# Performance work log

Hardware: AMD Instinct MI355X
Metric: run time of the kernel (lower is better)

The kernel has to match this reference:

```python
import jax, jax.numpy as jnp
import numpy as np

N_NODES = 100000
N_EDGES = 1600000
N_GRAPHS = 512
NFEAT = 64
HIDDEN = 128
NTARGETS = 16
TIME_DIM = 128
NLAYERS = 3  # conv1 + 2 extra convs


def setup_inputs() -> dict:
    key = jax.random.key(0)
    ks = jax.random.split(key, 12)
    x = jax.random.normal(ks[0], (N_NODES, NFEAT), dtype=jnp.float32)
    edge_index = jax.random.randint(ks[1], (2, N_EDGES), 0, N_NODES, dtype=jnp.int64)
    t_embedding = jax.random.normal(ks[2], (N_NODES, TIME_DIM), dtype=jnp.float32)
    batch = jnp.sort(jax.random.randint(ks[3], (N_NODES,), 0, N_GRAPHS, dtype=jnp.int64))
    s = lambda k, shp, fan_in: jax.random.normal(k, shp, jnp.float32) * (1.0 / np.sqrt(fan_in))
    Wt = s(ks[4], (TIME_DIM, HIDDEN), TIME_DIM)
    bt = jnp.zeros((HIDDEN,), jnp.float32)
    W1 = s(ks[5], (NFEAT, HIDDEN), NFEAT)
    b1 = jnp.zeros((HIDDEN,), jnp.float32)
    Ws = s(ks[6], (NLAYERS - 1, HIDDEN, HIDDEN), HIDDEN)
    bs = jnp.zeros((NLAYERS - 1, HIDDEN), jnp.float32)
    Wo = s(ks[7], (HIDDEN, NTARGETS), HIDDEN)
    bo = jnp.zeros((NTARGETS,), jnp.float32)
    return {"x": x, "edge_index": edge_index, "t_embedding": t_embedding,
            "batch": batch, "Wt": Wt, "bt": bt, "W1": W1, "b1": b1,
            "Ws": Ws, "bs": bs, "Wo": Wo, "bo": bo}


def _gcn_conv(h, src, dst, norm, W, b, n_nodes):
    # PyG GCNConv: h' = scatter_add(norm * (h @ W)[src] -> dst) + b
    h = h @ W                                   # [N, out]
    msg = h[src] * norm[:, None]                # [E+N, out]
    agg = jax.ops.segment_sum(msg, dst, num_segments=n_nodes)
    return agg + b


def reference(x, edge_index, t_embedding, batch, Wt, bt, W1, b1, Ws, bs, Wo, bo):
    n = x.shape[0]
    # add self-loops (static shapes)
    loop = jnp.arange(n, dtype=edge_index.dtype)
    src = jnp.concatenate([edge_index[0], loop])
    dst = jnp.concatenate([edge_index[1], loop])
    # symmetric normalization D^-1/2 (A+I) D^-1/2
    deg = jax.ops.segment_sum(jnp.ones(dst.shape[0], x.dtype), dst, num_segments=n)
    dinv = jnp.where(deg > 0, jax.lax.rsqrt(deg), 0.0)
    norm = dinv[src] * dinv[dst]                # [E+N]

    t_emb = jax.nn.relu(t_embedding @ Wt + bt)  # time_mlp
    h = jax.nn.relu(_gcn_conv(x, src, dst, norm, W1, b1, n)) + t_emb
    for i in range(Ws.shape[0]):
        h = jax.nn.relu(_gcn_conv(h, src, dst, norm, Ws[i], bs[i], n))

    # global mean pool over graphs
    gsum = jax.ops.segment_sum(h, batch, num_segments=N_GRAPHS)
    cnt = jax.ops.segment_sum(jnp.ones(n, h.dtype), batch, num_segments=N_GRAPHS)
    pooled = gsum / jnp.maximum(cnt, 1.0)[:, None]
    return pooled @ Wo + bo
```

## Files before the change

### kernel.cpp

```cpp
#include <hip/hip_runtime.h>

#define N_NODES  100000
#define N_EDGES  1600000
#define N_GRAPHS 512
#define HID      128
#define NB       196
#define NCHUNK   196
#define CHUNK    8192
#define ECAP     512

typedef unsigned int  uint;
typedef unsigned char uchar;
typedef unsigned short ushort;
typedef __attribute__((ext_vector_type(8))) short  short8;
typedef __attribute__((ext_vector_type(4))) float  f32x4;
typedef __attribute__((ext_vector_type(2))) float  f32x2;

__device__ inline float bflo(uint u) { return __uint_as_float(u << 16); }
__device__ inline float bfhi(uint u) { return __uint_as_float(u & 0xffff0000u); }
__device__ inline ushort f2bf(float f) {
    uint u = __float_as_uint(f);
    return (ushort)((u + 0x7fffu + ((u >> 16) & 1u)) >> 16);
}
__device__ inline uint pk(float a, float b) {
    return (uint)f2bf(a) | ((uint)f2bf(b) << 16);
}

__device__ inline void acc16_fp8(uint4 hv, float w, float* a) {
    f32x2 p;
    p = __builtin_amdgcn_cvt_pk_f32_fp8((int)hv.x, false); a[0]  += w * p.x; a[1]  += w * p.y;
    p = __builtin_amdgcn_cvt_pk_f32_fp8((int)hv.x, true);  a[2]  += w * p.x; a[3]  += w * p.y;
    p = __builtin_amdgcn_cvt_pk_f32_fp8((int)hv.y, false); a[4]  += w * p.x; a[5]  += w * p.y;
    p = __builtin_amdgcn_cvt_pk_f32_fp8((int)hv.y, true);  a[6]  += w * p.x; a[7]  += w * p.y;
    p = __builtin_amdgcn_cvt_pk_f32_fp8((int)hv.z, false); a[8]  += w * p.x; a[9]  += w * p.y;
    p = __builtin_amdgcn_cvt_pk_f32_fp8((int)hv.z, true);  a[10] += w * p.x; a[11] += w * p.y;
    p = __builtin_amdgcn_cvt_pk_f32_fp8((int)hv.w, false); a[12] += w * p.x; a[13] += w * p.y;
    p = __builtin_amdgcn_cvt_pk_f32_fp8((int)hv.w, true);  a[14] += w * p.x; a[15] += w * p.y;
}

__global__ __launch_bounds__(256)
void prep_kernel(const float* __restrict__ Wt, const float* __restrict__ W1,
                 const float* __restrict__ Ws, ushort* __restrict__ packed,
                 const int* __restrict__ batch, int* __restrict__ gstart,
                 const float* __restrict__ temb, ushort* __restrict__ tembb) {
    int b = blockIdx.x;
    int t = threadIdx.x;
    if (b < 224) {
        int tid = b * 256 + t;
        const float* src; int p; ushort* dst;
        if (tid < 16384)      { src = Wt;         p = tid;         dst = packed; }
        else if (tid < 24576) { src = W1;         p = tid - 16384; dst = packed + 16384; }
        else if (tid < 40960) { src = Ws;         p = tid - 24576; dst = packed + 24576; }
        else                  { src = Ws + 16384; p = tid - 40960; dst = packed + 40960; }
        int j  = p & 7;
        int L  = (p >> 3) & 63;
        int cb = (p >> 9) & 7;
        int s  = p >> 12;
        int k  = s * 32 + (L >> 4) * 8 + j;
        int n  = cb * 16 + (L & 15);
        dst[p] = f2bf(src[k * 128 + n]);
    } else if (b < 615) {
        int i = (b - 224) * 256 + t;
        if (i >= N_NODES) return;
        int bb = batch[i];
        int prev = (i == 0) ? -1 : batch[i - 1];
        for (int g = prev + 1; g <= bb; ++g) gstart[g] = i;
        if (i == N_NODES - 1) {
            for (int g = bb + 1; g <= N_GRAPHS; ++g) gstart[g] = N_NODES;
        }
    } else {
        long i = ((long)(b - 615) * 256 + t) * 16;
#pragma unroll
        for (int k = 0; k < 4; ++k) {
            float4 f = *(const float4*)(temb + i + k * 4);
            uint2 o; o.x = pk(f.x, f.y); o.y = pk(f.z, f.w);
            *(uint2*)(tembb + i + k * 4) = o;
        }
    }
}


__global__ __launch_bounds__(256)
void hist_chunks(const int* __restrict__ dst, int* __restrict__ chunk_hist) {
    __shared__ int h[NB];
    int c = blockIdx.x, t = threadIdx.x;
    if (t < NB) h[t] = 0;
    __syncthreads();
    const int4* d4 = (const int4*)dst;
#pragma unroll
    for (int k = 0; k < 8; ++k) {
        int i4 = c * (CHUNK / 4) + k * 256 + t;
        if (i4 < N_EDGES / 4) {
            int4 d = d4[i4];
            atomicAdd(&h[d.x >> 9], 1);
            atomicAdd(&h[d.y >> 9], 1);
            atomicAdd(&h[d.z >> 9], 1);
            atomicAdd(&h[d.w >> 9], 1);
        }
    }
    __syncthreads();
    if (t < NB) chunk_hist[c * NB + t] = h[t];
}

__global__ __launch_bounds__(256)
void scan_chunks(const int* __restrict__ chunk_hist, int* __restrict__ cbase,
                 int* __restrict__ bstart, int* __restrict__ row_ptr) {
    __shared__ int sc[256];
    int t = threadIdx.x;
    int tot = 0;
    if (t < NB)
        for (int c = 0; c < NCHUNK; ++c) tot += chunk_hist[c * NB + t];
    sc[t] = (t < NB) ? tot : 0;
    __syncthreads();
    for (int off = 1; off < 256; off <<= 1) {
        int x = (t >= off) ? sc[t - off] : 0;
        __syncthreads();
        sc[t] += x;
        __syncthreads();
    }
    int excl = sc[t] - ((t < NB) ? tot : 0);
    if (t < NB) {
        bstart[t] = excl;
        int run = excl;
        for (int c = 0; c < NCHUNK; ++c) {
            cbase[c * NB + t] = run;
            run += chunk_hist[c * NB + t];
        }
    }
    if (t == 0) { bstart[NB] = N_EDGES; row_ptr[N_NODES] = N_EDGES; }
}

__global__ __launch_bounds__(256)
void scatter_coarse(const int* __restrict__ src, const int* __restrict__ dst,
                    const int* __restrict__ cbase, uint* __restrict__ tmp) {
    __shared__ int cur[NB];
    int c = blockIdx.x, t = threadIdx.x;
    if (t < NB) cur[t] = cbase[c * NB + t];
    __syncthreads();
    const int4* s4p = (const int4*)src;
    const int4* d4p = (const int4*)dst;
#pragma unroll
    for (int k = 0; k < 8; ++k) {
        int i4 = c * (CHUNK / 4) + k * 256 + t;
        if (i4 < N_EDGES / 4) {
            int4 s = s4p[i4];
            int4 d = d4p[i4];
            int p;
            p = atomicAdd(&cur[d.x >> 9], 1); tmp[p] = (uint)s.x | (((uint)(d.x & 511)) << 17);
            p = atomicAdd(&cur[d.y >> 9], 1); tmp[p] = (uint)s.y | (((uint)(d.y & 511)) << 17);
            p = atomicAdd(&cur[d.z >> 9], 1); tmp[p] = (uint)s.z | (((uint)(d.z & 511)) << 17);
            p = atomicAdd(&cur[d.w >> 9], 1); tmp[p] = (uint)s.w | (((uint)(d.w & 511)) << 17);
        }
    }
}

__global__ __launch_bounds__(256)
void csr_fine(const uint* __restrict__ tmp, const int* __restrict__ bstart,
              int* __restrict__ row_ptr, float* __restrict__ dinv,
              int* __restrict__ edge, const float* __restrict__ x,
              uchar* __restrict__ xb8) {
    __shared__ int   cnt[512];
    __shared__ float dvloc[512];
    __shared__ int   ps[256];
    int b = blockIdx.x, t = threadIdx.x;
    int node0 = b << 9;
    int ncnt = min(512, N_NODES - node0);
    int s = bstart[b], e = bstart[b + 1];
    cnt[t] = 0; cnt[t + 256] = 0;
    __syncthreads();
    for (int i = s + t; i < e; i += 256) atomicAdd(&cnt[tmp[i] >> 17], 1);
    __syncthreads();
    int c0 = cnt[2 * t], c1 = cnt[2 * t + 1];
    int pair = c0 + c1;
    ps[t] = pair;
    __syncthreads();
    for (int off = 1; off < 256; off <<= 1) {
        int v = (t >= off) ? ps[t - off] : 0;
        __syncthreads();
        ps[t] += v;
        __syncthreads();
    }
    int ep = ps[t] - pair;
    int p0 = s + ep, p1 = s + ep + c0;
    float dv0 = rsqrtf((float)(c0 + 1));
    float dv1 = rsqrtf((float)(c1 + 1));
    int n0 = node0 + 2 * t;
    if (2 * t < ncnt)     { row_ptr[n0]     = p0; dinv[n0]     = dv0; }
    if (2 * t + 1 < ncnt) { row_ptr[n0 + 1] = p1; dinv[n0 + 1] = dv1; }
    dvloc[2 * t] = dv0; dvloc[2 * t + 1] = dv1;
    cnt[2 * t] = p0; cnt[2 * t + 1] = p1;
    __syncthreads();
    for (int i = s + t; i < e; i += 256) {
        uint rec = tmp[i];
        int p = atomicAdd(&cnt[rec >> 17], 1);
        edge[p] = (int)(rec & 0x1FFFFu);
    }
    for (int idx = t; idx < ncnt * 16; idx += 256) {
        int row = idx >> 4, q = idx & 15;
        float4 f = ((const float4*)(x + (size_t)(node0 + row) * 64))[q];
        float d = dvloc[row];
        int w = __builtin_amdgcn_cvt_pk_fp8_f32(f.x * d, f.y * d, 0, false);
        w     = __builtin_amdgcn_cvt_pk_fp8_f32(f.z * d, f.w * d, w, true);
        *(uint*)(xb8 + (size_t)(node0 + row) * 64 + q * 4) = (uint)w;
    }
}

template <int K, bool TEMB, bool OUT8, bool SCALEOUT>
__global__ __launch_bounds__(256)
void fused_conv(const void* __restrict__ Hv, const int* __restrict__ rp,
                const int* __restrict__ edge, const float* __restrict__ dinv,
                const ushort* __restrict__ Wp, const float* __restrict__ bias,
                const ushort* __restrict__ tembb, const ushort* __restrict__ Wtp,
                const float* __restrict__ bias_t, void* __restrict__ Ov, int ntiles) {
    constexpr int LPR  = K / 16;
    constexpr int G    = 64 / LPR;
    constexpr int RPG  = 16 / G;
    constexpr int U    = 8;
    constexpr int LROW = 136;
    __shared__ __align__(16) ushort sA[4][16 * LROW];
    __shared__ uint sE[4][ECAP];
    const int wave = threadIdx.x >> 6;
    const int lane = threadIdx.x & 63;
    const int tile = blockIdx.x * 4 + wave;
    if (tile >= ntiles) return;
    const int row0 = tile * 16;
    const int g  = lane / LPR;
    const int fq = lane % LPR;
    ushort* myA = sA[wave];
    const uchar* H8 = (const uchar*)Hv;

    int   rpv = rp[row0 + ((lane < 17) ? lane : 16)];
    float dvv = dinv[row0 + ((lane < 16) ? lane : 15)];

    const int s0   = __shfl(rpv, 0);
    const int e15  = __shfl(rpv, 16);
    const int ecnt = e15 - s0;
    uint* sEw = sE[wave];
    for (int i = lane; i < ecnt && i < ECAP; i += 64)
        sEw[i] = ((const uint*)edge)[s0 + i];

    auto phase1 = [&](auto eload) {
        for (int rr = 0; rr < RPG; ++rr) {
            int r = g * RPG + rr;
            int v = row0 + r;
            int s = __shfl(rpv, r), e = __shfl(rpv, r + 1);
            float a[16];
            {
                uint4 xv = *(const uint4*)(H8 + (size_t)v * K + fq * 16);
                f32x2 p;
                p = __builtin_amdgcn_cvt_pk_f32_fp8((int)xv.x, false); a[0]  = p.x; a[1]  = p.y;
                p = __builtin_amdgcn_cvt_pk_f32_fp8((int)xv.x, true);  a[2]  = p.x; a[3]  = p.y;
                p = __builtin_amdgcn_cvt_pk_f32_fp8((int)xv.y, false); a[4]  = p.x; a[5]  = p.y;
                p = __builtin_amdgcn_cvt_pk_f32_fp8((int)xv.y, true);  a[6]  = p.x; a[7]  = p.y;
                p = __builtin_amdgcn_cvt_pk_f32_fp8((int)xv.z, false); a[8]  = p.x; a[9]  = p.y;
                p = __builtin_amdgcn_cvt_pk_f32_fp8((int)xv.z, true);  a[10] = p.x; a[11] = p.y;
                p = __builtin_amdgcn_cvt_pk_f32_fp8((int)xv.w, false); a[12] = p.x; a[13] = p.y;
                p = __builtin_amdgcn_cvt_pk_f32_fp8((int)xv.w, true);  a[14] = p.x; a[15] = p.y;
            }
            int iters = (e - s + U - 1) / U;
            int j = s;
            for (int i = 0; i < iters; ++i, j += U) {
                int sv[U]; float wv[U];
#pragma unroll
                for (int u = 0; u < U; ++u) {
                    int jv = j + u;
                    int jj = (jv < e) ? jv : e - 1;
                    sv[u] = eload(jj);
                    wv[u] = (jv < e) ? 1.0f : 0.0f;
                }
                uint4 hv[U];
#pragma unroll
                for (int u = 0; u < U; ++u)
                    hv[u] = *(const uint4*)(H8 + (size_t)sv[u] * K + fq * 16);
#pragma unroll
                for (int u = 0; u < U; ++u) acc16_fp8(hv[u], wv[u], a);
            }
            float dv = __shfl(dvv, r);
            uint4 o1, o2;
            o1.x = pk(a[0] * dv,  a[1] * dv);  o1.y = pk(a[2] * dv,  a[3] * dv);
            o1.z = pk(a[4] * dv,  a[5] * dv);  o1.w = pk(a[6] * dv,  a[7] * dv);
            o2.x = pk(a[8] * dv,  a[9] * dv);  o2.y = pk(a[10] * dv, a[11] * dv);
            o2.z = pk(a[12] * dv, a[13] * dv); o2.w = pk(a[14] * dv, a[15] * dv);
            *(uint4*)(myA + r * LROW + fq * 16)     = o1;
            *(uint4*)(myA + r * LROW + fq * 16 + 8) = o2;
        }
    };
    if (ecnt <= ECAP) {
        phase1([&](int jj) { return (int)sEw[jj - s0]; });
    } else {
        phase1([&](int jj) { return (int)((const uint*)edge)[jj]; });
    }

    const int m = lane & 15, q = lane >> 4;
    f32x4 acc[8];
#pragma unroll
    for (int cb = 0; cb < 8; ++cb) acc[cb] = {0.f, 0.f, 0.f, 0.f};
    constexpr int S = K / 32;
#pragma unroll
    for (int s = 0; s < S; ++s) {
        short8 av = *(const short8*)(myA + m * LROW + s * 32 + q * 8);
#pragma unroll
        for (int cb = 0; cb < 8; ++cb) {
            short8 b = *(const short8*)(Wp + (size_t)((s * 8 + cb) * 64 + lane) * 8);
            acc[cb] = __builtin_amdgcn_mfma_f32_16x16x32_bf16(av, b, acc[cb], 0, 0, 0);
        }
    }

    f32x4 acc2[TEMB ? 8 : 1];
    if constexpr (TEMB) {
#pragma unroll
        for (int cb = 0; cb < 8; ++cb) acc2[cb] = {0.f, 0.f, 0.f, 0.f};
        const ushort* Arow = tembb + (size_t)(row0 + m) * 128 + q * 8;
#pragma unroll
        for (int s2 = 0; s2 < 4; ++s2) {
            short8 av = *(const short8*)(Arow + s2 * 32);
#pragma unroll
            for (int cb = 0; cb < 8; ++cb) {
                short8 b = *(const short8*)(Wtp + (size_t)((s2 * 8 + cb) * 64 + lane) * 8);
                acc2[cb] = __builtin_amdgcn_mfma_f32_16x16x32_bf16(av, b, acc2[cb], 0, 0, 0);
            }
        }
    }

    float dsc[4];
    if constexpr (SCALEOUT) {
#pragma unroll
        for (int r = 0; r < 4; ++r) dsc[r] = __shfl(dvv, q * 4 + r);
    }
    if constexpr (!OUT8) {
        ushort* Ob = (ushort*)Ov;
#pragma unroll
        for (int cb = 0; cb < 8; ++cb) {
            int colc = cb * 16 + m;
            float bv = bias[colc];
            float bt2 = TEMB ? bias_t[colc] : 0.f;
#pragma unroll
            for (int r = 0; r < 4; ++r) {
                int row = q * 4 + r;
                float v = fmaxf(acc[cb][r] + bv, 0.0f);
                if (TEMB) v += fmaxf(acc2[cb][r] + bt2, 0.0f);
                if (SCALEOUT) v *= dsc[r];
                myA[row * LROW + colc] = f2bf(v);
            }
        }
#pragma unroll
        for (int i = 0; i < 4; ++i) {
            int srow = i * 4 + (lane >> 4);
            int scol = (lane & 15) * 8;
            *(short8*)(Ob + (size_t)(row0 + srow) * 128 + scol) =
                *(const short8*)(myA + srow * LROW + scol);
        }
    } else {
        uchar* st8 = (uchar*)myA;
        uchar* Ob = (uchar*)Ov;
#pragma unroll
        for (int cb = 0; cb < 8; ++cb) {
            int colc = cb * 16 + m;
            float bv = bias[colc];
            float bt2 = TEMB ? bias_t[colc] : 0.f;
#pragma unroll
            for (int r = 0; r < 4; ++r) {
                int row = q * 4 + r;
                float v = fmaxf(acc[cb][r] + bv, 0.0f);
                if (TEMB) v += fmaxf(acc2[cb][r] + bt2, 0.0f);
                if (SCALEOUT) v *= dsc[r];
                int enc = __builtin_amdgcn_cvt_pk_fp8_f32(v, v, 0, false);
                st8[row * 136 + colc] = (uchar)(enc & 0xff);
            }
        }
#pragma unroll
        for (int i = 0; i < 4; ++i) {
            int idx = i * 64 + lane;
            int srow = idx >> 4;
            int soff = (idx & 15) * 8;
            *(uint2*)(Ob + (size_t)(row0 + srow) * 128 + soff) =
                *(const uint2*)(st8 + srow * 136 + soff);
        }
    }
}


__global__ void pool_out(const ushort* __restrict__ h, const int* __restrict__ gstart,
                         const float* __restrict__ Wo, const float* __restrict__ bo,
                         float* __restrict__ out) {
    int g = blockIdx.x;
    int t = threadIdx.x;
    int f4 = t & 31;
    int sl = t >> 5;
    int s = gstart[g], e = gstart[g + 1];
    float a0 = 0.f, a1 = 0.f, a2 = 0.f, a3 = 0.f;
    for (int i = s + sl; i < e; i += 8) {
        uint2 u = *(const uint2*)(h + (size_t)i * HID + f4 * 4);
        a0 += bflo(u.x); a1 += bfhi(u.x);
        a2 += bflo(u.y); a3 += bfhi(u.y);
    }
    __shared__ float red[256][4];
    __shared__ float P[128];
    red[t][0] = a0; red[t][1] = a1; red[t][2] = a2; red[t][3] = a3;
    __syncthreads();
    if (sl == 0) {
        for (int k = 1; k < 8; ++k) {
            a0 += red[f4 + 32 * k][0]; a1 += red[f4 + 32 * k][1];
            a2 += red[f4 + 32 * k][2]; a3 += red[f4 + 32 * k][3];
        }
        float c = (float)((e - s) < 1 ? 1 : (e - s));
        P[f4 * 4]     = a0 / c; P[f4 * 4 + 1] = a1 / c;
        P[f4 * 4 + 2] = a2 / c; P[f4 * 4 + 3] = a3 / c;
    }
    __syncthreads();
    if (t < 16) {
        float acc = bo[t];
        for (int k = 0; k < HID; ++k) acc += P[k] * Wo[k * 16 + t];
        out[g * 16 + t] = acc;
    }
}


extern "C" void kernel_launch(void* const* d_in, const int* in_sizes, int n_in,
                              void* d_out, int out_size, void* d_ws, size_t ws_size,
                              hipStream_t stream) {
    const float* x       = (const float*)d_in[0];
    const int*   ei      = (const int*)d_in[1];
    const float* temb_in = (const float*)d_in[2];
    const int*   batch   = (const int*)d_in[3];
    const float* Wt      = (const float*)d_in[4];
    const float* bt      = (const float*)d_in[5];
    const float* W1      = (const float*)d_in[6];
    const float* b1      = (const float*)d_in[7];
    const float* Ws      = (const float*)d_in[8];
    const float* bs      = (const float*)d_in[9];
    const float* Wo      = (const float*)d_in[10];
    const float* bo      = (const float*)d_in[11];
    float* out = (float*)d_out;

    const int N = N_NODES, E = N_EDGES;
    const int* src = ei;
    const int* dst = ei + E;

    char* p = (char*)d_ws;
    auto carve = [&](size_t bytes) -> void* {
        void* r = (void*)p;
        p += (bytes + 255) & ~(size_t)255;
        return r;
    };
    int*    row_ptr    = (int*)carve((size_t)(N + 1) * 4);
    float*  dinv       = (float*)carve((size_t)N * 4);
    int*    gstart     = (int*)carve((size_t)(N_GRAPHS + 1) * 4);
    ushort* packed     = (ushort*)carve((size_t)57344 * 2);
    int*    chunk_hist = (int*)carve((size_t)NCHUNK * NB * 4);
    int*    cbase      = (int*)carve((size_t)NCHUNK * NB * 4);
    int*    bstart     = (int*)carve((size_t)(NB + 1) * 4);
    uint*   tmp        = (uint*)carve((size_t)E * 4);
    int*    edge       = (int*)carve((size_t)E * 4);
    uchar*  xb8        = (uchar*)carve((size_t)(N + 16) * 64);
    ushort* tembb      = (ushort*)carve((size_t)N * 128 * 2);
    uchar*  H1f8       = (uchar*)carve((size_t)(N + 16) * 128);
    uchar*  H2f8       = (uchar*)carve((size_t)(N + 16) * 128);
    ushort* H3         = (ushort*)carve((size_t)N * 128 * 2);

    const ushort* Wtp  = packed;
    const ushort* W1p  = packed + 16384;
    const ushort* Ws0p = packed + 24576;
    const ushort* Ws1p = packed + 40960;

    const int ntiles = N / 16;
    const int gblk   = (ntiles + 3) / 4;

    prep_kernel<<<3740, 256, 0, stream>>>(Wt, W1, Ws, packed, batch, gstart,
                                          temb_in, tembb);

    hist_chunks<<<NCHUNK, 256, 0, stream>>>(dst, chunk_hist);
    scan_chunks<<<1, 256, 0, stream>>>(chunk_hist, cbase, bstart, row_ptr);
    scatter_coarse<<<NCHUNK, 256, 0, stream>>>(src, dst, cbase, tmp);
    csr_fine<<<NB, 256, 0, stream>>>(tmp, bstart, row_ptr, dinv, edge, x, xb8);

    fused_conv<64, true, true, true><<<gblk, 256, 0, stream>>>(
        xb8, row_ptr, edge, dinv, W1p, b1, tembb, Wtp, bt, H1f8, ntiles);
    fused_conv<128, false, true, true><<<gblk, 256, 0, stream>>>(
        H1f8, row_ptr, edge, dinv, Ws0p, bs, nullptr, nullptr, nullptr, H2f8, ntiles);
    fused_conv<128, false, false, false><<<gblk, 256, 0, stream>>>(
        H2f8, row_ptr, edge, dinv, Ws1p, bs + 128, nullptr, nullptr, nullptr, H3, ntiles);

    pool_out<<<N_GRAPHS, 256, 0, stream>>>(H3, gstart, Wo, bo, out);
}
```

Baseline: 367.9 us.

## Fuse pooling into last conv, merge histogram into prep, refine CSR buckets

Several changes land together. The edge histogram moves into the prep kernel, and the coarse bucket count grows from 196 to 782 buckets of 128 nodes. The single serial scan becomes a parallel two-level scan over a transposed layout. The last conv now reduces its tile rows per graph and accumulates them into a float pooled buffer with atomics, which removes the bf16 H3 write, the pool_out read and one launch. The cost is global atomic contention on pooled and more blocks in csr_fine, each using only half its threads.

```diff
diff --git a/kernel.cpp b/kernel.cpp
--- a/kernel.cpp
+++ b/kernel.cpp
@@ -4,7 +4,7 @@
 #define N_EDGES  1600000
 #define N_GRAPHS 512
 #define HID      128
-#define NB       196
+#define NB       782
 #define NCHUNK   196
 #define CHUNK    8192
 #define ECAP     512
@@ -42,23 +42,26 @@
 void prep_kernel(const float* __restrict__ Wt, const float* __restrict__ W1,
                  const float* __restrict__ Ws, ushort* __restrict__ packed,
                  const int* __restrict__ batch, int* __restrict__ gstart,
-                 const float* __restrict__ temb, ushort* __restrict__ tembb) {
+                 const float* __restrict__ temb, ushort* __restrict__ tembb,
+                 const int* __restrict__ dst, int* __restrict__ chunk_hist,
+                 float* __restrict__ pooled) {
+    __shared__ int h[NB];
     int b = blockIdx.x;
     int t = threadIdx.x;
     if (b < 224) {
         int tid = b * 256 + t;
-        const float* src; int p; ushort* dst;
-        if (tid < 16384)      { src = Wt;         p = tid;         dst = packed; }
-        else if (tid < 24576) { src = W1;         p = tid - 16384; dst = packed + 16384; }
-        else if (tid < 40960) { src = Ws;         p = tid - 24576; dst = packed + 24576; }
-        else                  { src = Ws + 16384; p = tid - 40960; dst = packed + 40960; }
+        const float* src; int p; ushort* dstp;
+        if (tid < 16384)      { src = Wt;         p = tid;         dstp = packed; }
+        else if (tid < 24576) { src = W1;         p = tid - 16384; dstp = packed + 16384; }
+        else if (tid < 40960) { src = Ws;         p = tid - 24576; dstp = packed + 24576; }
+        else                  { src = Ws + 16384; p = tid - 40960; dstp = packed + 40960; }
         int j  = p & 7;
         int L  = (p >> 3) & 63;
         int cb = (p >> 9) & 7;
         int s  = p >> 12;
         int k  = s * 32 + (L >> 4) * 8 + j;
         int n  = cb * 16 + (L & 15);
-        dst[p] = f2bf(src[k * 128 + n]);
+        dstp[p] = f2bf(src[k * 128 + n]);
     } else if (b < 615) {
         int i = (b - 224) * 256 + t;
         if (i >= N_NODES) return;
@@ -68,7 +71,7 @@
         if (i == N_NODES - 1) {
             for (int g = bb + 1; g <= N_GRAPHS; ++g) gstart[g] = N_NODES;
         }
-    } else {
+    } else if (b < 3740) {
         long i = ((long)(b - 615) * 256 + t) * 16;
 #pragma unroll
         for (int k = 0; k < 4; ++k) {
@@ -76,41 +79,61 @@
             uint2 o; o.x = pk(f.x, f.y); o.y = pk(f.z, f.w);
             *(uint2*)(tembb + i + k * 4) = o;
         }
-    }
-}
-
-
-__global__ __launch_bounds__(256)
-void hist_chunks(const int* __restrict__ dst, int* __restrict__ chunk_hist) {
-    __shared__ int h[NB];
-    int c = blockIdx.x, t = threadIdx.x;
-    if (t < NB) h[t] = 0;
-    __syncthreads();
-    const int4* d4 = (const int4*)dst;
-#pragma unroll
-    for (int k = 0; k < 8; ++k) {
-        int i4 = c * (CHUNK / 4) + k * 256 + t;
-        if (i4 < N_EDGES / 4) {
-            int4 d = d4[i4];
-            atomicAdd(&h[d.x >> 9], 1);
-            atomicAdd(&h[d.y >> 9], 1);
-            atomicAdd(&h[d.z >> 9], 1);
-            atomicAdd(&h[d.w >> 9], 1);
-        }
-    }
-    __syncthreads();
-    if (t < NB) chunk_hist[c * NB + t] = h[t];
-}
-
-__global__ __launch_bounds__(256)
-void scan_chunks(const int* __restrict__ chunk_hist, int* __restrict__ cbase,
-                 int* __restrict__ bstart, int* __restrict__ row_ptr) {
+    } else if (b < 3936) {
+        int c = b - 3740;
+        for (int i = t; i < NB; i += 256) h[i] = 0;
+        __syncthreads();
+        const int4* d4 = (const int4*)dst;
+#pragma unroll
+        for (int k = 0; k < 8; ++k) {
+            int i4 = c * (CHUNK / 4) + k * 256 + t;
+            if (i4 < N_EDGES / 4) {
+                int4 d = d4[i4];
+                atomicAdd(&h[d.x >> 7], 1);
+                atomicAdd(&h[d.y >> 7], 1);
+                atomicAdd(&h[d.z >> 7], 1);
+                atomicAdd(&h[d.w >> 7], 1);
+            }
+        }
+        __syncthreads();
+        for (int i = t; i < NB; i += 256) chunk_hist[c * NB + i] = h[i];
+    } else {
+        pooled[(b - 3936) * 256 + t] = 0.f;
+    }
+}
+
+
+__global__ __launch_bounds__(256)
+void scanA(const int* __restrict__ chunk_hist, int* __restrict__ cbaseT,
+           int* __restrict__ btotal) {
+    __shared__ int sc[256];
+    int b = blockIdx.x, t = threadIdx.x;
+    int v = (t < NCHUNK) ? chunk_hist[t * NB + b] : 0;
+    sc[t] = v;
+    __syncthreads();
+    for (int off = 1; off < 256; off <<= 1) {
+        int x = (t >= off) ? sc[t - off] : 0;
+        __syncthreads();
+        sc[t] += x;
+        __syncthreads();
+    }
+    if (t < NCHUNK) cbaseT[b * NCHUNK + t] = sc[t] - v;
+    if (t == 255) btotal[b] = sc[255];
+}
+
+__global__ __launch_bounds__(256)
+void scanB(const int* __restrict__ btotal, int* __restrict__ bstart,
+           int* __restrict__ row_ptr) {
     __shared__ int sc[256];
     int t = threadIdx.x;
-    int tot = 0;
-    if (t < NB)
-        for (int c = 0; c < NCHUNK; ++c) tot += chunk_hist[c * NB + t];
-    sc[t] = (t < NB) ? tot : 0;
+    int v[4]; int sum = 0;
+#pragma unroll
+    for (int k = 0; k < 4; ++k) {
+        int idx = t * 4 + k;
+        v[k] = (idx < NB) ? btotal[idx] : 0;
+        sum += v[k];
+    }
+    sc[t] = sum;
     __syncthreads();
     for (int off = 1; off < 256; off <<= 1) {
         int x = (t >= off) ? sc[t - off] : 0;
@@ -118,24 +141,23 @@
         sc[t] += x;
         __syncthreads();
     }
-    int excl = sc[t] - ((t < NB) ? tot : 0);
-    if (t < NB) {
-        bstart[t] = excl;
-        int run = excl;
-        for (int c = 0; c < NCHUNK; ++c) {
-            cbase[c * NB + t] = run;
-            run += chunk_hist[c * NB + t];
-        }
+    int run = sc[t] - sum;
+#pragma unroll
+    for (int k = 0; k < 4; ++k) {
+        int idx = t * 4 + k;
+        if (idx < NB) bstart[idx] = run;
+        run += v[k];
     }
     if (t == 0) { bstart[NB] = N_EDGES; row_ptr[N_NODES] = N_EDGES; }
 }
 
 __global__ __launch_bounds__(256)
 void scatter_coarse(const int* __restrict__ src, const int* __restrict__ dst,
-                    const int* __restrict__ cbase, uint* __restrict__ tmp) {
+                    const int* __restrict__ cbaseT, const int* __restrict__ bstart,
+                    uint* __restrict__ tmp) {
     __shared__ int cur[NB];
     int c = blockIdx.x, t = threadIdx.x;
-    if (t < NB) cur[t] = cbase[c * NB + t];
+    for (int i = t; i < NB; i += 256) cur[i] = cbaseT[i * NCHUNK + c] + bstart[i];
     __syncthreads();
     const int4* s4p = (const int4*)src;
     const int4* d4p = (const int4*)dst;
@@ -146,10 +168,10 @@
             int4 s = s4p[i4];
             int4 d = d4p[i4];
             int p;
-            p = atomicAdd(&cur[d.x >> 9], 1); tmp[p] = (uint)s.x | (((uint)(d.x & 511)) << 17);
-            p = atomicAdd(&cur[d.y >> 9], 1); tmp[p] = (uint)s.y | (((uint)(d.y & 511)) << 17);
-            p = atomicAdd(&cur[d.z >> 9], 1); tmp[p] = (uint)s.z | (((uint)(d.z & 511)) << 17);
-            p = atomicAdd(&cur[d.w >> 9], 1); tmp[p] = (uint)s.w | (((uint)(d.w & 511)) << 17);
+            p = atomicAdd(&cur[d.x >> 7], 1); tmp[p] = (uint)s.x | (((uint)(d.x & 127)) << 17);
+            p = atomicAdd(&cur[d.y >> 7], 1); tmp[p] = (uint)s.y | (((uint)(d.y & 127)) << 17);
+            p = atomicAdd(&cur[d.z >> 7], 1); tmp[p] = (uint)s.z | (((uint)(d.z & 127)) << 17);
+            p = atomicAdd(&cur[d.w >> 7], 1); tmp[p] = (uint)s.w | (((uint)(d.w & 127)) << 17);
         }
     }
 }
@@ -159,36 +181,33 @@
               int* __restrict__ row_ptr, float* __restrict__ dinv,
               int* __restrict__ edge, const float* __restrict__ x,
               uchar* __restrict__ xb8) {
-    __shared__ int   cnt[512];
-    __shared__ float dvloc[512];
-    __shared__ int   ps[256];
+    __shared__ int   cnt[128];
+    __shared__ float dvloc[128];
+    __shared__ int   ps[128];
     int b = blockIdx.x, t = threadIdx.x;
-    int node0 = b << 9;
-    int ncnt = min(512, N_NODES - node0);
+    int node0 = b << 7;
+    int ncnt = min(128, N_NODES - node0);
     int s = bstart[b], e = bstart[b + 1];
-    cnt[t] = 0; cnt[t + 256] = 0;
+    if (t < 128) cnt[t] = 0;
     __syncthreads();
     for (int i = s + t; i < e; i += 256) atomicAdd(&cnt[tmp[i] >> 17], 1);
     __syncthreads();
-    int c0 = cnt[2 * t], c1 = cnt[2 * t + 1];
-    int pair = c0 + c1;
-    ps[t] = pair;
-    __syncthreads();
-    for (int off = 1; off < 256; off <<= 1) {
-        int v = (t >= off) ? ps[t - off] : 0;
-        __syncthreads();
-        ps[t] += v;
-        __syncthreads();
-    }
-    int ep = ps[t] - pair;
-    int p0 = s + ep, p1 = s + ep + c0;
-    float dv0 = rsqrtf((float)(c0 + 1));
-    float dv1 = rsqrtf((float)(c1 + 1));
-    int n0 = node0 + 2 * t;
-    if (2 * t < ncnt)     { row_ptr[n0]     = p0; dinv[n0]     = dv0; }
-    if (2 * t + 1 < ncnt) { row_ptr[n0 + 1] = p1; dinv[n0 + 1] = dv1; }
-    dvloc[2 * t] = dv0; dvloc[2 * t + 1] = dv1;
-    cnt[2 * t] = p0; cnt[2 * t + 1] = p1;
+    int c0 = (t < 128) ? cnt[t] : 0;
+    if (t < 128) ps[t] = c0;
+    __syncthreads();
+    for (int off = 1; off < 128; off <<= 1) {
+        int v = (t < 128 && t >= off) ? ps[t - off] : 0;
+        __syncthreads();
+        if (t < 128) ps[t] += v;
+        __syncthreads();
+    }
+    if (t < 128) {
+        int p0 = s + ps[t] - c0;
+        float dv = rsqrtf((float)(c0 + 1));
+        if (t < ncnt) { row_ptr[node0 + t] = p0; dinv[node0 + t] = dv; }
+        dvloc[t] = dv;
+        cnt[t] = p0;
+    }
     __syncthreads();
     for (int i = s + t; i < e; i += 256) {
         uint rec = tmp[i];
@@ -205,13 +224,14 @@
     }
 }
 
-template <int K, bool TEMB, bool OUT8, bool SCALEOUT>
+template <int K, bool TEMB, bool OUT8, bool SCALEOUT, bool POOL>
 __global__ __launch_bounds__(256)
 void fused_conv(const void* __restrict__ Hv, const int* __restrict__ rp,
                 const int* __restrict__ edge, const float* __restrict__ dinv,
                 const ushort* __restrict__ Wp, const float* __restrict__ bias,
                 const ushort* __restrict__ tembb, const ushort* __restrict__ Wtp,
-                const float* __restrict__ bias_t, void* __restrict__ Ov, int ntiles) {
+                const float* __restrict__ bias_t, void* __restrict__ Ov,
+                const int* __restrict__ batchp, float* __restrict__ pooled, int ntiles) {
     constexpr int LPR  = K / 16;
     constexpr int G    = 64 / LPR;
     constexpr int RPG  = 16 / G;
@@ -260,20 +280,22 @@
             int iters = (e - s + U - 1) / U;
             int j = s;
             for (int i = 0; i < iters; ++i, j += U) {
-                int sv[U]; float wv[U];
+                int sv[U];
 #pragma unroll
                 for (int u = 0; u < U; ++u) {
                     int jv = j + u;
                     int jj = (jv < e) ? jv : e - 1;
                     sv[u] = eload(jj);
-                    wv[u] = (jv < e) ? 1.0f : 0.0f;
                 }
                 uint4 hv[U];
 #pragma unroll
                 for (int u = 0; u < U; ++u)
                     hv[u] = *(const uint4*)(H8 + (size_t)sv[u] * K + fq * 16);
 #pragma unroll
-                for (int u = 0; u < U; ++u) acc16_fp8(hv[u], wv[u], a);
+                for (int u = 0; u < U; ++u) {
+                    float w = (j + u < e) ? 1.0f : 0.0f;
+                    acc16_fp8(hv[u], w, a);
+                }
             }
             float dv = __shfl(dvv, r);
             uint4 o1, o2;
@@ -343,12 +365,30 @@
                 myA[row * LROW + colc] = f2bf(v);
             }
         }
-#pragma unroll
-        for (int i = 0; i < 4; ++i) {
-            int srow = i * 4 + (lane >> 4);
-            int scol = (lane & 15) * 8;
-            *(short8*)(Ob + (size_t)(row0 + srow) * 128 + scol) =
-                *(const short8*)(myA + srow * LROW + scol);
+        if constexpr (!POOL) {
+#pragma unroll
+            for (int i = 0; i < 4; ++i) {
+                int srow = i * 4 + (lane >> 4);
+                int scol = (lane & 15) * 8;
+                *(short8*)(Ob + (size_t)(row0 + srow) * 128 + scol) =
+                    *(const short8*)(myA + srow * LROW + scol);
+            }
+        } else {
+            int gidv = (lane < 16) ? batchp[row0 + lane] : 0;
+            int colb = lane * 2;
+            float p0 = 0.f, p1 = 0.f;
+#pragma unroll
+            for (int r = 0; r < 16; ++r) {
+                uint u = *(const uint*)(myA + r * LROW + colb);
+                p0 += bflo(u); p1 += bfhi(u);
+                int curg  = __shfl(gidv, r);
+                int nextg = (r < 15) ? __shfl(gidv, r + 1) : -1;
+                if (nextg != curg) {
+                    atomicAdd(&pooled[curg * 128 + colb],     p0);
+                    atomicAdd(&pooled[curg * 128 + colb + 1], p1);
+                    p0 = 0.f; p1 = 0.f;
+                }
+            }
         }
     } else {
         uchar* st8 = (uchar*)myA;
@@ -380,39 +420,19 @@
 }
 
 
-__global__ void pool_out(const ushort* __restrict__ h, const int* __restrict__ gstart,
-                         const float* __restrict__ Wo, const float* __restrict__ bo,
-                         float* __restrict__ out) {
-    int g = blockIdx.x;
-    int t = threadIdx.x;
-    int f4 = t & 31;
-    int sl = t >> 5;
-    int s = gstart[g], e = gstart[g + 1];
-    float a0 = 0.f, a1 = 0.f, a2 = 0.f, a3 = 0.f;
-    for (int i = s + sl; i < e; i += 8) {
-        uint2 u = *(const uint2*)(h + (size_t)i * HID + f4 * 4);
-        a0 += bflo(u.x); a1 += bfhi(u.x);
-        a2 += bflo(u.y); a3 += bfhi(u.y);
-    }
-    __shared__ float red[256][4];
-    __shared__ float P[128];
-    red[t][0] = a0; red[t][1] = a1; red[t][2] = a2; red[t][3] = a3;
-    __syncthreads();
-    if (sl == 0) {
-        for (int k = 1; k < 8; ++k) {
-            a0 += red[f4 + 32 * k][0]; a1 += red[f4 + 32 * k][1];
-            a2 += red[f4 + 32 * k][2]; a3 += red[f4 + 32 * k][3];
-        }
-        float c = (float)((e - s) < 1 ? 1 : (e - s));
-        P[f4 * 4]     = a0 / c; P[f4 * 4 + 1] = a1 / c;
-        P[f4 * 4 + 2] = a2 / c; P[f4 * 4 + 3] = a3 / c;
-    }
-    __syncthreads();
-    if (t < 16) {
-        float acc = bo[t];
-        for (int k = 0; k < HID; ++k) acc += P[k] * Wo[k * 16 + t];
-        out[g * 16 + t] = acc;
-    }
+__global__ __launch_bounds__(256)
+void head_kernel(const float* __restrict__ pooled, const int* __restrict__ gstart,
+                 const float* __restrict__ Wo, const float* __restrict__ bo,
+                 float* __restrict__ out) {
+    int g  = blockIdx.x * 16 + (threadIdx.x >> 4);
+    int tg = threadIdx.x & 15;
+    if (g >= N_GRAPHS) return;
+    int c = gstart[g + 1] - gstart[g];
+    float inv = 1.0f / (float)(c < 1 ? 1 : c);
+    float acc = bo[tg];
+    for (int k = 0; k < HID; ++k)
+        acc += pooled[g * 128 + k] * inv * Wo[k * 16 + tg];
+    out[g * 16 + tg] = acc;
 }
 
 
@@ -448,7 +468,8 @@
     int*    gstart     = (int*)carve((size_t)(N_GRAPHS + 1) * 4);
     ushort* packed     = (ushort*)carve((size_t)57344 * 2);
     int*    chunk_hist = (int*)carve((size_t)NCHUNK * NB * 4);
-    int*    cbase      = (int*)carve((size_t)NCHUNK * NB * 4);
+    int*    cbaseT     = (int*)carve((size_t)NB * NCHUNK * 4);
+    int*    btotal     = (int*)carve((size_t)NB * 4);
     int*    bstart     = (int*)carve((size_t)(NB + 1) * 4);
     uint*   tmp        = (uint*)carve((size_t)E * 4);
     int*    edge       = (int*)carve((size_t)E * 4);
@@ -456,7 +477,7 @@
     ushort* tembb      = (ushort*)carve((size_t)N * 128 * 2);
     uchar*  H1f8       = (uchar*)carve((size_t)(N + 16) * 128);
     uchar*  H2f8       = (uchar*)carve((size_t)(N + 16) * 128);
-    ushort* H3         = (ushort*)carve((size_t)N * 128 * 2);
+    float*  pooled     = (float*)carve((size_t)N_GRAPHS * 128 * 4);
 
     const ushort* Wtp  = packed;
     const ushort* W1p  = packed + 16384;
@@ -466,20 +487,23 @@
     const int ntiles = N / 16;
     const int gblk   = (ntiles + 3) / 4;
 
-    prep_kernel<<<3740, 256, 0, stream>>>(Wt, W1, Ws, packed, batch, gstart,
-                                          temb_in, tembb);
-
-    hist_chunks<<<NCHUNK, 256, 0, stream>>>(dst, chunk_hist);
-    scan_chunks<<<1, 256, 0, stream>>>(chunk_hist, cbase, bstart, row_ptr);
-    scatter_coarse<<<NCHUNK, 256, 0, stream>>>(src, dst, cbase, tmp);
+    prep_kernel<<<4192, 256, 0, stream>>>(Wt, W1, Ws, packed, batch, gstart,
+                                          temb_in, tembb, dst, chunk_hist, pooled);
+
+    scanA<<<NB, 256, 0, stream>>>(chunk_hist, cbaseT, btotal);
+    scanB<<<1, 256, 0, stream>>>(btotal, bstart, row_ptr);
+    scatter_coarse<<<NCHUNK, 256, 0, stream>>>(src, dst, cbaseT, bstart, tmp);
     csr_fine<<<NB, 256, 0, stream>>>(tmp, bstart, row_ptr, dinv, edge, x, xb8);
 
-    fused_conv<64, true, true, true><<<gblk, 256, 0, stream>>>(
-        xb8, row_ptr, edge, dinv, W1p, b1, tembb, Wtp, bt, H1f8, ntiles);
-    fused_conv<128, false, true, true><<<gblk, 256, 0, stream>>>(
-        H1f8, row_ptr, edge, dinv, Ws0p, bs, nullptr, nullptr, nullptr, H2f8, ntiles);
-    fused_conv<128, false, false, false><<<gblk, 256, 0, stream>>>(
-        H2f8, row_ptr, edge, dinv, Ws1p, bs + 128, nullptr, nullptr, nullptr, H3, ntiles);
-
-    pool_out<<<N_GRAPHS, 256, 0, stream>>>(H3, gstart, Wo, bo, out);
-}
+    fused_conv<64, true, true, true, false><<<gblk, 256, 0, stream>>>(
+        xb8, row_ptr, edge, dinv, W1p, b1, tembb, Wtp, bt, H1f8,
+        nullptr, nullptr, ntiles);
+    fused_conv<128, false, true, true, false><<<gblk, 256, 0, stream>>>(
+        H1f8, row_ptr, edge, dinv, Ws0p, bs, nullptr, nullptr, nullptr, H2f8,
+        nullptr, nullptr, ntiles);
+    fused_conv<128, false, false, false, true><<<gblk, 256, 0, stream>>>(
+        H2f8, row_ptr, edge, dinv, Ws1p, bs + 128, nullptr, nullptr, nullptr, nullptr,
+        batch, pooled, ntiles);
+
+    head_kernel<<<32, 256, 0, stream>>>(pooled, gstart, Wo, bo, out);
+}
```

Measured after the change: 347.1 us. 5.6% less time.
